# Optimization experiments

Measured on AMD Instinct MI355X. Metric: run time of the kernel, lower is better.

## Reference

```python
import jax, jax.numpy as jnp
import numpy as np
from jax import lax

B, N, D, E, P, K, H = 32, 512, 512, 8, 96, 25, 4
PAD = 12  # conv padding so length is preserved


def setup_inputs() -> dict:
    key = jax.random.key(0)
    ks = jax.random.split(key, 16)
    s = 0.05  # weight scale to keep softmax/cosine well-conditioned
    x = jax.random.normal(ks[0], (B, N, D), dtype=jnp.float32)
    router = jax.random.normal(ks[1], (1, E, D), dtype=jnp.float32)
    Wq = jax.random.normal(ks[2], (D, D), dtype=jnp.float32) * s
    bq = jax.random.normal(ks[3], (D,), dtype=jnp.float32) * s
    Wk = jax.random.normal(ks[4], (D, D), dtype=jnp.float32) * s
    bk = jax.random.normal(ks[5], (D,), dtype=jnp.float32) * s
    Wv = jax.random.normal(ks[6], (D, D), dtype=jnp.float32) * s
    bv = jax.random.normal(ks[7], (D,), dtype=jnp.float32) * s
    Wo = jax.random.normal(ks[8], (D, D), dtype=jnp.float32) * s
    bo = jax.random.normal(ks[9], (D,), dtype=jnp.float32) * s
    Wc = jax.random.normal(ks[10], (E, 2, K), dtype=jnp.float32) * s  # E experts' Conv1d(2,1,25) stacked as out-channels
    bc = jax.random.normal(ks[11], (E,), dtype=jnp.float32) * s
    Wp = jax.random.normal(ks[12], (E, D, P), dtype=jnp.float32) * s  # E experts' Linear(D,P), stored (in,out)
    bp = jax.random.normal(ks[13], (E, P), dtype=jnp.float32) * s
    return {"x": x, "router": router, "Wq": Wq, "bq": bq, "Wk": Wk, "bk": bk,
            "Wv": Wv, "bv": bv, "Wo": Wo, "bo": bo, "Wc": Wc, "bc": bc,
            "Wp": Wp, "bp": bp}


def _forward(x, router, Wq, bq, Wk, bk, Wv, bv, Wo, bo, Wc, bc, Wp, bp):
    b, n, d = x.shape
    e = router.shape[1]
    dk = d // H
    r = jnp.broadcast_to(router, (b, e, d))
    # multi-head attention: queries=router slots, keys/values=x (dropout = identity at eval)
    q = (r @ Wq + bq).reshape(b, e, H, dk)
    k = (x @ Wk + bk).reshape(b, n, H, dk)
    v = (x @ Wv + bv).reshape(b, n, H, dk)
    scale = 1.0 / jnp.sqrt(jnp.asarray(dk, x.dtype))
    scores = jnp.einsum('blhe,bshe->bhls', q, k)  # [b,H,e,n]
    A = jax.nn.softmax(scale * scores, axis=-1)
    att = jnp.einsum('bhls,bshd->blhd', A, v).reshape(b, e, d)
    att = att @ Wo + bo  # [b,e,d]
    # cosine-similarity routing score, mapped to (1+pi)/2
    dot = jnp.einsum('bed,bnd->ben', att, x)
    norm_a = jnp.linalg.norm(att, axis=2, keepdims=True)          # [b,e,1]
    norm_x = jnp.linalg.norm(x, axis=2)[:, None, :]                # [b,1,n]
    score = (1.0 + dot / (norm_a * norm_x)) / 2.0                  # [b,e,n]
    idx = jnp.argmax(score, axis=1)                                # [b,n] expert per token
    z = jnp.take_along_axis(att, idx[:, :, None], axis=1)          # [b,n,d]
    result = jnp.stack([x, z], axis=-2).reshape(b * n, 2, d)       # [bn,2,d]
    # run all E expert convs at once (experts stacked as output channels)
    conv_out = lax.conv_general_dilated(
        result, Wc, window_strides=(1,), padding=[(PAD, PAD)],
        dimension_numbers=('NCH', 'OIH', 'NCH')) + bc[None, :, None]  # [bn,E,d]
    lin = jnp.einsum('nel,elp->nep', conv_out, Wp) + bp[None]         # [bn,E,P]
    flat_idx = idx.reshape(-1)
    out = jnp.take_along_axis(lin, flat_idx[:, None, None], axis=1)[:, 0, :]
    return out.reshape(b, n, P)


def reference(x, router, Wq, bq, Wk, bk, Wv, bv, Wo, bo, Wc, bc, Wp, bp):
    return _forward(x, router, Wq, bq, Wk, bk, Wv, bv, Wo, bo, Wc, bc, Wp, bp)
```

## Files before the change

### kernel.cpp

```cpp
#include <hip/hip_runtime.h>
#include <hip/hip_bf16.h>

#define B_ 32
#define N_ 512
#define D_ 512
#define E_ 8
#define P_ 96
#define KC 25
#define H_ 4
#define DK 128
#define HE 32
#define BN 16384

typedef short short8 __attribute__((ext_vector_type(8)));
typedef float f32x4 __attribute__((ext_vector_type(4)));

#define OCNT  4096
#define OS2   4352
#define OM    5120
#define OC    21504
#define OA    21536
#define OATT  676896
#define OTOK  807968
#define OWEFF 939040
#define OZC   1332256
#define OUP   1356832
#define OA1   5551136

__device__ __forceinline__ float b2f(short s) {
  unsigned u = ((unsigned)(unsigned short)s) << 16;
  return __builtin_bit_cast(float, u);
}
__device__ __forceinline__ unsigned short f2b(float f) {
  return __builtin_bit_cast(unsigned short, __float2bfloat16(f));
}

__global__ __launch_bounds__(256) void k_head(const float* __restrict__ router,
        const float* __restrict__ Wq, const float* __restrict__ bq,
        const float* __restrict__ Wk, const float* __restrict__ bk,
        const float* __restrict__ Wp, const float* __restrict__ Wc,
        float* __restrict__ M, float* __restrict__ c,
        int* __restrict__ cnt, float* __restrict__ s2,
        __hip_bfloat16* __restrict__ weff) {
  __shared__ float sm[5824];
  int bid = blockIdx.x;
  int tid = threadIdx.x;
  if (bid < 64) {
    float* rs = sm;
    float* ps = sm + 512;
    float* qs = sm + 768;
    int he = bid >> 1, ch = bid & 1;
    int h = he >> 3, e = he & 7;
    for (int i = tid; i < 512; i += 256) rs[i] = router[e * D_ + i];
    __syncthreads();
    {
      int j = tid & 127, dh = tid >> 7;
      const float* wq = Wq + h * 128 + j;
      float acc = 0.f;
      for (int d = dh * 256; d < dh * 256 + 256; d += 4) {
        acc = fmaf(rs[d], wq[d * D_], acc);
        acc = fmaf(rs[d + 1], wq[(d + 1) * D_], acc);
        acc = fmaf(rs[d + 2], wq[(d + 2) * D_], acc);
        acc = fmaf(rs[d + 3], wq[(d + 3) * D_], acc);
      }
      ps[dh * 128 + j] = acc;
    }
    __syncthreads();
    if (tid < 128) qs[tid] = ps[tid] + ps[128 + tid] + bq[h * 128 + tid];
    __syncthreads();
    {
      int d0 = ch * 256 + tid;
      const float* wrow = Wk + d0 * D_ + h * 128;
      float acc = 0.f;
      for (int jj = 0; jj < 128; jj += 4) {
        float4 wv = *(const float4*)(wrow + jj);
        acc = fmaf(wv.x, qs[jj], acc);
        acc = fmaf(wv.y, qs[jj + 1], acc);
        acc = fmaf(wv.z, qs[jj + 2], acc);
        acc = fmaf(wv.w, qs[jj + 3], acc);
      }
      M[he * D_ + d0] = acc;
    }
    if (ch == 0 && tid < 64) {
      float s = qs[tid] * bk[h * 128 + tid] + qs[tid + 64] * bk[h * 128 + tid + 64];
#pragma unroll
      for (int off = 32; off; off >>= 1) s += __shfl_xor(s, off);
      if (tid == 0) c[he] = s;
    }
  } else if (bid < 192) {
    float* T = sm;
    float* wcs = sm + 5760;
    int eb = bid - 64;
    int e = eb >> 4, mc = eb & 15;
    int lo = mc * 32 - 12;
    for (int idx = tid; idx < 56 * 24; idx += 256) {
      int lp = idx / 24, p4 = (idx - lp * 24) * 4;
      int l = lo + lp;
      float4 v = {0.f, 0.f, 0.f, 0.f};
      if (l >= 0 && l < D_) v = *(const float4*)(Wp + (e * D_ + l) * P_ + p4);
      T[p4 * 60 + lp] = v.x; T[(p4 + 1) * 60 + lp] = v.y;
      T[(p4 + 2) * 60 + lp] = v.z; T[(p4 + 3) * 60 + lp] = v.w;
    }
    if (tid < 50) wcs[tid] = Wc[e * 2 * KC + tid];
    __syncthreads();
    int m = tid & 31, pg = tid >> 5;
#pragma unroll
    for (int j = 0; j < 2; ++j)
      for (int k2 = 0; k2 < 12; ++k2) {
        int p = pg * 12 + k2;
        float acc = 0.f;
#pragma unroll
        for (int k = 0; k < KC; ++k)
          acc = fmaf(wcs[j * 25 + k], T[p * 60 + m - k + 24], acc);
        weff[(((e * 2 + j) * P_ + p) << 9) + mc * 32 + m] = __float2bfloat16(acc);
      }
  } else {
    int e = bid - 192;
    if (bid == 192) cnt[tid] = 0;
    if (tid < 192) {
      int p = tid % 96, lg = tid / 96;
      float s = 0.f;
      const float* wp = Wp + e * D_ * P_ + p;
      for (int l = lg * 256; l < lg * 256 + 256; ++l) s += wp[l * P_];
      sm[lg * 96 + p] = s;
    }
    __syncthreads();
    if (tid < 96) s2[e * 96 + tid] = sm[tid] + sm[96 + tid];
  }
}

__global__ __launch_bounds__(128) void k_logits(const float* __restrict__ x,
        const float* __restrict__ M, float* __restrict__ A0,
        float* __restrict__ A1) {
  __shared__ float xs[64 * 132];
  __shared__ float Ms[32 * 132];
  int dh = blockIdx.x & 1;
  int nt8 = (blockIdx.x >> 1) & 7;
  int b = blockIdx.x >> 4;
  int tid = threadIdx.x;
  const float* xb = x + (b * N_ + nt8 * 64) * D_ + dh * 256;
  const float* Mb = M + dh * 256;
  float acc[4][4] = {{0.f}};
  for (int kc = 0; kc < 2; ++kc) {
    for (int idx = tid; idx < 2048; idx += 128) {
      int r = idx >> 5, c4 = (idx & 31) * 4;
      *(float4*)(xs + r * 132 + c4) = *(const float4*)(xb + r * D_ + kc * 128 + c4);
    }
    for (int idx = tid; idx < 1024; idx += 128) {
      int r = idx >> 5, c4 = (idx & 31) * 4;
      *(float4*)(Ms + r * 132 + c4) = *(const float4*)(Mb + r * D_ + kc * 128 + c4);
    }
    __syncthreads();
    int nt = tid & 15, ht = tid >> 4;
#pragma unroll 4
    for (int d4 = 0; d4 < 128; d4 += 4) {
      float4 xv[4], mv[4];
#pragma unroll
      for (int i = 0; i < 4; ++i)
        xv[i] = *(const float4*)(xs + (nt + 16 * i) * 132 + d4);
#pragma unroll
      for (int j = 0; j < 4; ++j)
        mv[j] = *(const float4*)(Ms + (ht + 8 * j) * 132 + d4);
#pragma unroll
      for (int i = 0; i < 4; ++i)
#pragma unroll
        for (int j = 0; j < 4; ++j) {
          float s = acc[i][j];
          s = fmaf(xv[i].x, mv[j].x, s);
          s = fmaf(xv[i].y, mv[j].y, s);
          s = fmaf(xv[i].z, mv[j].z, s);
          s = fmaf(xv[i].w, mv[j].w, s);
          acc[i][j] = s;
        }
    }
    __syncthreads();
  }
  int nt = tid & 15, ht = tid >> 4;
  float* Ad = dh ? A1 : A0;
#pragma unroll
  for (int j = 0; j < 4; ++j) {
    int he = ht + 8 * j;
#pragma unroll
    for (int i = 0; i < 4; ++i)
      Ad[(b * HE + he) * N_ + nt8 * 64 + nt + 16 * i] = acc[i][j];
  }
}

__global__ __launch_bounds__(512) void k_u3(const float* __restrict__ x,
        const float* __restrict__ A0, const float* __restrict__ A1,
        const float* __restrict__ c, float* __restrict__ up) {
  __shared__ float As[64 * 33];
  __shared__ float mS[32], sS[32];
  int nq = blockIdx.x, b = blockIdx.y;
  int tid = threadIdx.x;
  const float scale = 0.08838834764831845f;
  {
    int wv = tid >> 6, lane = tid & 63;
    int he = wv * 4 + (lane >> 4);
    int l16 = lane & 15;
    const float* r0 = A0 + (b * HE + he) * N_;
    const float* r1 = A1 + (b * HE + he) * N_;
    float cc = c[he];
    float v[32];
    float m = -1e30f;
#pragma unroll
    for (int k = 0; k < 32; ++k) {
      int n = l16 + k * 16;
      float vv = scale * (r0[n] + r1[n] + cc);
      v[k] = vv;
      m = fmaxf(m, vv);
    }
    m = fmaxf(m, __shfl_xor(m, 1)); m = fmaxf(m, __shfl_xor(m, 2));
    m = fmaxf(m, __shfl_xor(m, 4)); m = fmaxf(m, __shfl_xor(m, 8));
    float s = 0.f;
#pragma unroll
    for (int k = 0; k < 32; ++k) s += expf(v[k] - m);
    s += __shfl_xor(s, 1); s += __shfl_xor(s, 2);
    s += __shfl_xor(s, 4); s += __shfl_xor(s, 8);
    if (l16 == 0) { mS[he] = m; sS[he] = 1.0f / s; }
  }
  __syncthreads();
  for (int idx = tid; idx < 64 * 32; idx += 512) {
    int n = idx & 63, he = idx >> 6;
    int gn = nq * 64 + n;
    float vv = scale * (A0[(b * HE + he) * N_ + gn] + A1[(b * HE + he) * N_ + gn]
                        + c[he]);
    As[n * 33 + he] = expf(vv - mS[he]) * sS[he];
  }
  __syncthreads();
  int dq = tid & 127, hg = tid >> 7;
  const float* xb = x + (b * N_ + nq * 64) * D_ + dq * 4;
  float acc[8][4];
#pragma unroll
  for (int j = 0; j < 8; ++j)
#pragma unroll
    for (int k = 0; k < 4; ++k) acc[j][k] = 0.f;
  for (int n = 0; n < 64; ++n) {
    float4 xv = *(const float4*)(xb + n * D_);
    const float* ar = As + n * 33 + hg * 8;
#pragma unroll
    for (int j = 0; j < 8; ++j) {
      float a = ar[j];
      acc[j][0] = fmaf(a, xv.x, acc[j][0]);
      acc[j][1] = fmaf(a, xv.y, acc[j][1]);
      acc[j][2] = fmaf(a, xv.z, acc[j][2]);
      acc[j][3] = fmaf(a, xv.w, acc[j][3]);
    }
  }
  float* o = up + (((b * 8 + nq) * HE) + hg * 8) * D_ + dq * 4;
#pragma unroll
  for (int j = 0; j < 8; ++j) {
    float4 v; v.x = acc[j][0]; v.y = acc[j][1]; v.z = acc[j][2]; v.w = acc[j][3];
    *(float4*)(o + j * D_) = v;
  }
}

__global__ __launch_bounds__(512) void k_vo3(const float* __restrict__ up,
        const float* __restrict__ Wv, const float* __restrict__ bv,
        const float* __restrict__ Wo, const float* __restrict__ bo,
        float* __restrict__ att) {
  __shared__ float us[4 * 512];
  __shared__ float part[4 * 512];
  __shared__ float ap_s[512];
  int b = blockIdx.x >> 3, e = blockIdx.x & 7;
  int tid = threadIdx.x;
  for (int idx = tid; idx < 4 * 128; idx += 512) {
    int h = idx >> 7, d4 = (idx & 127) * 4;
    const float* base = up + ((b * 8) * HE + h * 8 + e) * D_ + d4;
    float4 s = {0.f, 0.f, 0.f, 0.f};
#pragma unroll
    for (int nq = 0; nq < 8; ++nq) {
      float4 v = *(const float4*)(base + nq * HE * D_);
      s.x += v.x; s.y += v.y; s.z += v.z; s.w += v.w;
    }
    *(float4*)(us + h * 512 + d4) = s;
  }
  __syncthreads();
  {
    int cch = tid >> 7, j = tid & 127;
    int i0 = j * 4;
    int h = j >> 5;
    const float* ur = us + h * 512;
    const float* wv = Wv + i0;
    float4 acc = {0.f, 0.f, 0.f, 0.f};
    int d0 = cch * 128;
#pragma unroll 4
    for (int d = d0; d < d0 + 128; ++d) {
      float4 wq = *(const float4*)(wv + d * D_);
      float a = ur[d];
      acc.x = fmaf(a, wq.x, acc.x);
      acc.y = fmaf(a, wq.y, acc.y);
      acc.z = fmaf(a, wq.z, acc.z);
      acc.w = fmaf(a, wq.w, acc.w);
    }
    *(float4*)(part + cch * 512 + i0) = acc;
  }
  __syncthreads();
  ap_s[tid] = part[tid] + part[512 + tid] + part[1024 + tid] + part[1536 + tid]
              + bv[tid];
  __syncthreads();
  {
    int cch = tid >> 7, j = tid & 127;
    int o0 = j * 4;
    const float* wo = Wo + o0;
    float4 acc = {0.f, 0.f, 0.f, 0.f};
    int i0 = cch * 128;
#pragma unroll 4
    for (int i = i0; i < i0 + 128; ++i) {
      float4 wq = *(const float4*)(wo + i * D_);
      float a = ap_s[i];
      acc.x = fmaf(a, wq.x, acc.x);
      acc.y = fmaf(a, wq.y, acc.y);
      acc.z = fmaf(a, wq.z, acc.z);
      acc.w = fmaf(a, wq.w, acc.w);
    }
    *(float4*)(part + cch * 512 + o0) = acc;
  }
  __syncthreads();
  att[(b * E_ + e) * D_ + tid] = part[tid] + part[512 + tid] + part[1024 + tid]
                                 + part[1536 + tid] + bo[tid];
}

__global__ __launch_bounds__(256) void k_route2(const float* __restrict__ x,
        const float* __restrict__ att, const __hip_bfloat16* __restrict__ weff,
        const float* __restrict__ s2, const float* __restrict__ bc,
        const float* __restrict__ bp, int* __restrict__ cnt,
        int* __restrict__ tok, float* __restrict__ zc) {
  __shared__ float att_s[8 * D_];
  __shared__ float rn[8];
  __shared__ float red[4][520];
  __shared__ int blist[8][32];
  __shared__ int bcnt[8];
  int b = blockIdx.x >> 4, tile = blockIdx.x & 15;
  for (int idx = threadIdx.x; idx < 1024; idx += 256)
    *(float4*)(att_s + idx * 4) = *(const float4*)(att + b * E_ * D_ + idx * 4);
  if (threadIdx.x < 8) bcnt[threadIdx.x] = 0;
  __syncthreads();
  {
    int e = threadIdx.x >> 5, l = threadIdx.x & 31;
    float s = 0.f;
    for (int d0 = l; d0 < D_; d0 += 32) {
      float v = att_s[e * D_ + d0];
      s = fmaf(v, v, s);
    }
#pragma unroll
    for (int off = 16; off; off >>= 1) s += __shfl_xor(s, off);
    if (l == 0) rn[e] = 1.0f / sqrtf(s);
  }
  __syncthreads();
  int w = threadIdx.x >> 6, lane = threadIdx.x & 63;
  int e2 = lane & 7, ch = lane >> 3;
  float* rw = red[w];
  for (int i = 0; i < 8; ++i) {
    int t = b * N_ + tile * 32 + w * 8 + i;
    const float* xp = x + t * D_ + lane * 8;
    float4 xa = *(const float4*)xp;
    float4 xb4 = *(const float4*)(xp + 4);
    float p[8];
#pragma unroll
    for (int e = 0; e < 8; ++e) {
      const float* apt = att_s + e * D_ + lane * 8;
      float4 a0 = *(const float4*)apt;
      float4 a1 = *(const float4*)(apt + 4);
      float s = a0.x * xa.x;
      s = fmaf(a0.y, xa.y, s); s = fmaf(a0.z, xa.z, s); s = fmaf(a0.w, xa.w, s);
      s = fmaf(a1.x, xb4.x, s); s = fmaf(a1.y, xb4.y, s);
      s = fmaf(a1.z, xb4.z, s); s = fmaf(a1.w, xb4.w, s);
      p[e] = s;
    }
#pragma unroll
    for (int e = 0; e < 8; ++e) rw[e * 65 + lane] = p[e];
    float s = 0.f;
#pragma unroll
    for (int k = 0; k < 8; ++k) s += rw[e2 * 65 + ch * 8 + k];
    s += __shfl_xor(s, 8); s += __shfl_xor(s, 16); s += __shfl_xor(s, 32);
    float sc = s * rn[e2];
    int be = e2;
#pragma unroll
    for (int off = 1; off < 8; off <<= 1) {
      float o = __shfl_xor(sc, off);
      int oe = __shfl_xor(be, off);
      if (o > sc || (o == sc && oe < be)) { sc = o; be = oe; }
    }
    if (lane == 0) {
      int slot = atomicAdd(&bcnt[be], 1);
      blist[be][slot] = t;
    }
  }
  __syncthreads();
  {
    int e = threadIdx.x >> 5, r = threadIdx.x & 31;
    int ce = bcnt[e];
    int gs = 0;
    if (r == 0 && ce > 0) gs = atomicAdd(&cnt[e * 32], ce);
    gs = __shfl(gs, (threadIdx.x & 63) & 32);
    for (int k2 = r; k2 < ce; k2 += 32) tok[e * BN + gs + k2] = blist[e][k2];
  }
  int grp = threadIdx.x >> 4, l16 = threadIdx.x & 15;
  for (int r = 0; r < 3; ++r) {
    int P = tile * 48 + r * 16 + grp;
    int ez = P / 96, p = P - ez * 96;
    const short* wrow = (const short*)weff + (((ez * 2 + 1) * P_ + p) << 9);
    const float* arow = att_s + ez * D_;
    float acc = 0.f;
#pragma unroll
    for (int seg = 0; seg < 4; ++seg) {
      int d = seg * 128 + l16 * 8;
      short8 w8 = *(const short8*)(wrow + d);
      const float* a8 = arow + d;
      acc = fmaf(a8[0], b2f(w8[0]), acc); acc = fmaf(a8[1], b2f(w8[1]), acc);
      acc = fmaf(a8[2], b2f(w8[2]), acc); acc = fmaf(a8[3], b2f(w8[3]), acc);
      acc = fmaf(a8[4], b2f(w8[4]), acc); acc = fmaf(a8[5], b2f(w8[5]), acc);
      acc = fmaf(a8[6], b2f(w8[6]), acc); acc = fmaf(a8[7], b2f(w8[7]), acc);
    }
    acc += __shfl_xor(acc, 1); acc += __shfl_xor(acc, 2);
    acc += __shfl_xor(acc, 4); acc += __shfl_xor(acc, 8);
    if (l16 == 0)
      zc[(b * E_ + ez) * P_ + p] = acc + bc[ez] * s2[ez * 96 + p] + bp[ez * 96 + p];
  }
}

__global__ __launch_bounds__(256) void k_final(const float* __restrict__ x,
        const __hip_bfloat16* __restrict__ weff, const float* __restrict__ zc,
        const int* __restrict__ cnt, const int* __restrict__ tok,
        float* __restrict__ out) {
  __shared__ __align__(16) unsigned short xsb[32 * 520];
  __shared__ int toks[32];
  int g = blockIdx.x;
  int cl_e[E_], bs[E_ + 1];
  bs[0] = 0;
#pragma unroll
  for (int e = 0; e < E_; ++e) {
    cl_e[e] = cnt[e * 32];
    bs[e + 1] = bs[e] + ((cl_e[e] + 31) >> 5);
  }
  if (g >= bs[E_]) return;
  int e = 0;
#pragma unroll
  for (int k = 1; k < E_; ++k) if (g >= bs[k]) e = k;
  int base = (g - bs[e]) * 32;
  int cnt_e = cl_e[e];
  int cl = cnt_e - base; if (cl > 32) cl = 32;
  int tid = threadIdx.x;
  if (tid < 32) toks[tid] = (tid < cl) ? tok[e * BN + base + tid] : tok[e * BN + base];
  __syncthreads();
  for (int idx = tid; idx < 32 * 128; idx += 256) {
    int r = idx >> 7, c4 = (idx & 127) * 4;
    float4 v = *(const float4*)(x + toks[r] * D_ + c4);
    ushort4 u4;
    u4.x = f2b(v.x); u4.y = f2b(v.y); u4.z = f2b(v.z); u4.w = f2b(v.w);
    *(ushort4*)(xsb + r * 520 + c4) = u4;
  }
  __syncthreads();
  int wave = tid >> 6, lane = tid & 63;
  int mw = wave & 1, nw = wave >> 1;
  int m16 = lane & 15, quad = lane >> 4;
  const short* w0 = (const short*)(weff + (e * 2 + 0) * P_ * D_);
  f32x4 acc[3];
#pragma unroll
  for (int nt = 0; nt < 3; ++nt) acc[nt] = (f32x4){0.f, 0.f, 0.f, 0.f};
  const short* arow = (const short*)xsb + (mw * 16 + m16) * 520 + quad * 8;
  const short* brow = w0 + (nw * 48 + m16) * D_ + quad * 8;
  for (int kt = 0; kt < 16; ++kt) {
    int koff = kt * 32;
    short8 a = *(const short8*)(arow + koff);
#pragma unroll
    for (int nt = 0; nt < 3; ++nt) {
      short8 bf = *(const short8*)(brow + nt * 16 * D_ + koff);
      acc[nt] = __builtin_amdgcn_mfma_f32_16x16x32_bf16(a, bf, acc[nt], 0, 0, 0);
    }
  }
#pragma unroll
  for (int nt = 0; nt < 3; ++nt)
#pragma unroll
    for (int rr = 0; rr < 4; ++rr) {
      int row = mw * 16 + quad * 4 + rr;
      if (row < cl) {
        int tg = toks[row];
        int bb = tg >> 9;
        int p = nw * 48 + nt * 16 + m16;
        out[tg * P_ + p] = acc[nt][rr] + zc[(bb * E_ + e) * P_ + p];
      }
    }
}

extern "C" void kernel_launch(void* const* d_in, const int* in_sizes, int n_in,
                              void* d_out, int out_size, void* d_ws, size_t ws_size,
                              hipStream_t stream) {
  const float* x      = (const float*)d_in[0];
  const float* router = (const float*)d_in[1];
  const float* Wq     = (const float*)d_in[2];
  const float* bq     = (const float*)d_in[3];
  const float* Wk     = (const float*)d_in[4];
  const float* bk     = (const float*)d_in[5];
  const float* Wv     = (const float*)d_in[6];
  const float* bv     = (const float*)d_in[7];
  const float* Wo     = (const float*)d_in[8];
  const float* bo     = (const float*)d_in[9];
  const float* Wc     = (const float*)d_in[10];
  const float* bc     = (const float*)d_in[11];
  const float* Wp     = (const float*)d_in[12];
  const float* bp     = (const float*)d_in[13];
  float* out = (float*)d_out;
  float* w = (float*)d_ws;

  int*   cnt  = (int*)(w + OCNT);
  float* s2   = w + OS2;
  float* M    = w + OM;
  float* c    = w + OC;
  float* A0   = w + OA;
  float* A1   = w + OA1;
  float* att  = w + OATT;
  int*   tok  = (int*)(w + OTOK);
  __hip_bfloat16* weff = (__hip_bfloat16*)(w + OWEFF);
  float* zc   = w + OZC;
  float* up   = w + OUP;

  k_head<<<200, 256, 0, stream>>>(router, Wq, bq, Wk, bk, Wp, Wc, M, c, cnt, s2, weff);
  k_logits<<<512, 128, 0, stream>>>(x, M, A0, A1);
  k_u3<<<dim3(8, 32), 512, 0, stream>>>(x, A0, A1, c, up);
  k_vo3<<<256, 512, 0, stream>>>(up, Wv, bv, Wo, bo, att);
  k_route2<<<512, 256, 0, stream>>>(x, att, weff, s2, bc, bp, cnt, tok, zc);
  k_final<<<520, 256, 0, stream>>>(x, weff, zc, cnt, tok, out);
}
```

Measured before the change: 223.2 us.

## Split V/O projection into two kernels that reuse weight loads across experts

The fused per-(batch,expert) V and O projection kernel is replaced by two kernels, each handling all 8 experts of a batch for one 128-column slice. Every Wv/Wo element loaded is now reused across 8 experts held in registers, so weight traffic drops roughly eightfold. The cost is an extra kernel launch and a round trip of the intermediate through global memory, which reuses the A0 workspace region. The grid also shrinks from 256 blocks to 128 blocks of 256 threads, which lowers occupancy.

```diff
diff --git a/kernel.cpp b/kernel.cpp
--- a/kernel.cpp
+++ b/kernel.cpp
@@ -255,70 +255,141 @@
   }
 }
 
-__global__ __launch_bounds__(512) void k_vo3(const float* __restrict__ up,
+__global__ __launch_bounds__(256) void k_voa(const float* __restrict__ up,
         const float* __restrict__ Wv, const float* __restrict__ bv,
-        const float* __restrict__ Wo, const float* __restrict__ bo,
-        float* __restrict__ att) {
-  __shared__ float us[4 * 512];
-  __shared__ float part[4 * 512];
-  __shared__ float ap_s[512];
-  int b = blockIdx.x >> 3, e = blockIdx.x & 7;
+        float* __restrict__ ap) {
+  __shared__ float us8[8][520];
+  __shared__ float pr[8192];
+  int b = blockIdx.x >> 2, h = blockIdx.x & 3;
   int tid = threadIdx.x;
-  for (int idx = tid; idx < 4 * 128; idx += 512) {
-    int h = idx >> 7, d4 = (idx & 127) * 4;
-    const float* base = up + ((b * 8) * HE + h * 8 + e) * D_ + d4;
+  for (int idx = tid; idx < 1024; idx += 256) {
+    int e = idx >> 7, d4 = (idx & 127) * 4;
+    const float* base = up + (((b * 8) * HE) + h * 8 + e) * D_ + d4;
     float4 s = {0.f, 0.f, 0.f, 0.f};
 #pragma unroll
     for (int nq = 0; nq < 8; ++nq) {
       float4 v = *(const float4*)(base + nq * HE * D_);
       s.x += v.x; s.y += v.y; s.z += v.z; s.w += v.w;
     }
-    *(float4*)(us + h * 512 + d4) = s;
+    *(float4*)(&us8[e][d4]) = s;
+  }
+  __syncthreads();
+  int cg = tid & 31, kk = tid >> 5;
+  int c0 = h * 128 + cg * 4;
+  float acc[8][4];
+#pragma unroll
+  for (int e = 0; e < 8; ++e)
+#pragma unroll
+    for (int j = 0; j < 4; ++j) acc[e][j] = 0.f;
+  for (int d = kk * 64; d < kk * 64 + 64; d += 4) {
+    float4 w0 = *(const float4*)(Wv + (d + 0) * D_ + c0);
+    float4 w1 = *(const float4*)(Wv + (d + 1) * D_ + c0);
+    float4 w2 = *(const float4*)(Wv + (d + 2) * D_ + c0);
+    float4 w3 = *(const float4*)(Wv + (d + 3) * D_ + c0);
+#pragma unroll
+    for (int e = 0; e < 8; ++e) {
+      float4 u = *(const float4*)(&us8[e][d]);
+      acc[e][0] = fmaf(u.x, w0.x, acc[e][0]);
+      acc[e][0] = fmaf(u.y, w1.x, acc[e][0]);
+      acc[e][0] = fmaf(u.z, w2.x, acc[e][0]);
+      acc[e][0] = fmaf(u.w, w3.x, acc[e][0]);
+      acc[e][1] = fmaf(u.x, w0.y, acc[e][1]);
+      acc[e][1] = fmaf(u.y, w1.y, acc[e][1]);
+      acc[e][1] = fmaf(u.z, w2.y, acc[e][1]);
+      acc[e][1] = fmaf(u.w, w3.y, acc[e][1]);
+      acc[e][2] = fmaf(u.x, w0.z, acc[e][2]);
+      acc[e][2] = fmaf(u.y, w1.z, acc[e][2]);
+      acc[e][2] = fmaf(u.z, w2.z, acc[e][2]);
+      acc[e][2] = fmaf(u.w, w3.z, acc[e][2]);
+      acc[e][3] = fmaf(u.x, w0.w, acc[e][3]);
+      acc[e][3] = fmaf(u.y, w1.w, acc[e][3]);
+      acc[e][3] = fmaf(u.z, w2.w, acc[e][3]);
+      acc[e][3] = fmaf(u.w, w3.w, acc[e][3]);
+    }
+  }
+#pragma unroll
+  for (int e = 0; e < 8; ++e) {
+    float4 v; v.x = acc[e][0]; v.y = acc[e][1]; v.z = acc[e][2]; v.w = acc[e][3];
+    *(float4*)(&pr[kk * 1024 + e * 128 + cg * 4]) = v;
   }
   __syncthreads();
   {
-    int cch = tid >> 7, j = tid & 127;
-    int i0 = j * 4;
-    int h = j >> 5;
-    const float* ur = us + h * 512;
-    const float* wv = Wv + i0;
-    float4 acc = {0.f, 0.f, 0.f, 0.f};
-    int d0 = cch * 128;
-#pragma unroll 4
-    for (int d = d0; d < d0 + 128; ++d) {
-      float4 wq = *(const float4*)(wv + d * D_);
-      float a = ur[d];
-      acc.x = fmaf(a, wq.x, acc.x);
-      acc.y = fmaf(a, wq.y, acc.y);
-      acc.z = fmaf(a, wq.z, acc.z);
-      acc.w = fmaf(a, wq.w, acc.w);
-    }
-    *(float4*)(part + cch * 512 + i0) = acc;
-  }
-  __syncthreads();
-  ap_s[tid] = part[tid] + part[512 + tid] + part[1024 + tid] + part[1536 + tid]
-              + bv[tid];
+    int e = tid >> 5, cc = (tid & 31) * 4;
+    float4 s = *(const float4*)(&pr[tid * 4]);
+#pragma unroll
+    for (int k = 1; k < 8; ++k) {
+      float4 p = *(const float4*)(&pr[k * 1024 + tid * 4]);
+      s.x += p.x; s.y += p.y; s.z += p.z; s.w += p.w;
+    }
+    float4 bb = *(const float4*)(bv + h * 128 + cc);
+    s.x += bb.x; s.y += bb.y; s.z += bb.z; s.w += bb.w;
+    *(float4*)(ap + (b * 8 + e) * D_ + h * 128 + cc) = s;
+  }
+}
+
+__global__ __launch_bounds__(256) void k_vob(const float* __restrict__ ap,
+        const float* __restrict__ Wo, const float* __restrict__ bo,
+        float* __restrict__ att) {
+  __shared__ float ap8[8][520];
+  __shared__ float pr[8192];
+  int b = blockIdx.x >> 2, cq = blockIdx.x & 3;
+  int tid = threadIdx.x;
+  for (int idx = tid; idx < 1024; idx += 256) {
+    int e = idx >> 7, i4 = (idx & 127) * 4;
+    *(float4*)(&ap8[e][i4]) = *(const float4*)(ap + (b * 8 + e) * D_ + i4);
+  }
+  __syncthreads();
+  int cg = tid & 31, kk = tid >> 5;
+  int c0 = cq * 128 + cg * 4;
+  float acc[8][4];
+#pragma unroll
+  for (int e = 0; e < 8; ++e)
+#pragma unroll
+    for (int j = 0; j < 4; ++j) acc[e][j] = 0.f;
+  for (int i = kk * 64; i < kk * 64 + 64; i += 4) {
+    float4 w0 = *(const float4*)(Wo + (i + 0) * D_ + c0);
+    float4 w1 = *(const float4*)(Wo + (i + 1) * D_ + c0);
+    float4 w2 = *(const float4*)(Wo + (i + 2) * D_ + c0);
+    float4 w3 = *(const float4*)(Wo + (i + 3) * D_ + c0);
+#pragma unroll
+    for (int e = 0; e < 8; ++e) {
+      float4 u = *(const float4*)(&ap8[e][i]);
+      acc[e][0] = fmaf(u.x, w0.x, acc[e][0]);
+      acc[e][0] = fmaf(u.y, w1.x, acc[e][0]);
+      acc[e][0] = fmaf(u.z, w2.x, acc[e][0]);
+      acc[e][0] = fmaf(u.w, w3.x, acc[e][0]);
+      acc[e][1] = fmaf(u.x, w0.y, acc[e][1]);
+      acc[e][1] = fmaf(u.y, w1.y, acc[e][1]);
+      acc[e][1] = fmaf(u.z, w2.y, acc[e][1]);
+      acc[e][1] = fmaf(u.w, w3.y, acc[e][1]);
+      acc[e][2] = fmaf(u.x, w0.z, acc[e][2]);
+      acc[e][2] = fmaf(u.y, w1.z, acc[e][2]);
+      acc[e][2] = fmaf(u.z, w2.z, acc[e][2]);
+      acc[e][2] = fmaf(u.w, w3.z, acc[e][2]);
+      acc[e][3] = fmaf(u.x, w0.w, acc[e][3]);
+      acc[e][3] = fmaf(u.y, w1.w, acc[e][3]);
+      acc[e][3] = fmaf(u.z, w2.w, acc[e][3]);
+      acc[e][3] = fmaf(u.w, w3.w, acc[e][3]);
+    }
+  }
+#pragma unroll
+  for (int e = 0; e < 8; ++e) {
+    float4 v; v.x = acc[e][0]; v.y = acc[e][1]; v.z = acc[e][2]; v.w = acc[e][3];
+    *(float4*)(&pr[kk * 1024 + e * 128 + cg * 4]) = v;
+  }
   __syncthreads();
   {
-    int cch = tid >> 7, j = tid & 127;
-    int o0 = j * 4;
-    const float* wo = Wo + o0;
-    float4 acc = {0.f, 0.f, 0.f, 0.f};
-    int i0 = cch * 128;
-#pragma unroll 4
-    for (int i = i0; i < i0 + 128; ++i) {
-      float4 wq = *(const float4*)(wo + i * D_);
-      float a = ap_s[i];
-      acc.x = fmaf(a, wq.x, acc.x);
-      acc.y = fmaf(a, wq.y, acc.y);
-      acc.z = fmaf(a, wq.z, acc.z);
-      acc.w = fmaf(a, wq.w, acc.w);
-    }
-    *(float4*)(part + cch * 512 + o0) = acc;
-  }
-  __syncthreads();
-  att[(b * E_ + e) * D_ + tid] = part[tid] + part[512 + tid] + part[1024 + tid]
-                                 + part[1536 + tid] + bo[tid];
+    int e = tid >> 5, cc = (tid & 31) * 4;
+    float4 s = *(const float4*)(&pr[tid * 4]);
+#pragma unroll
+    for (int k = 1; k < 8; ++k) {
+      float4 p = *(const float4*)(&pr[k * 1024 + tid * 4]);
+      s.x += p.x; s.y += p.y; s.z += p.z; s.w += p.w;
+    }
+    float4 bb = *(const float4*)(bo + cq * 128 + cc);
+    s.x += bb.x; s.y += bb.y; s.z += bb.z; s.w += bb.w;
+    *(float4*)(att + (b * E_ + e) * D_ + cq * 128 + cc) = s;
+  }
 }
 
 __global__ __launch_bounds__(256) void k_route2(const float* __restrict__ x,
@@ -515,11 +586,13 @@
   __hip_bfloat16* weff = (__hip_bfloat16*)(w + OWEFF);
   float* zc   = w + OZC;
   float* up   = w + OUP;
+  float* ap   = w + OA;
 
   k_head<<<200, 256, 0, stream>>>(router, Wq, bq, Wk, bk, Wp, Wc, M, c, cnt, s2, weff);
   k_logits<<<512, 128, 0, stream>>>(x, M, A0, A1);
   k_u3<<<dim3(8, 32), 512, 0, stream>>>(x, A0, A1, c, up);
-  k_vo3<<<256, 512, 0, stream>>>(up, Wv, bv, Wo, bo, att);
+  k_voa<<<128, 256, 0, stream>>>(up, Wv, bv, ap);
+  k_vob<<<128, 256, 0, stream>>>(ap, Wo, bo, att);
   k_route2<<<512, 256, 0, stream>>>(x, att, weff, s2, bc, bp, cnt, tok, zc);
   k_final<<<520, 256, 0, stream>>>(x, weff, zc, cnt, tok, out);
 }
```

After: 224.7 us. No clear change (+0.7%).

## Fuse last four kernels into one cooperative kernel with grid syncs

Applied to the files above, without the earlier changes.

Merges the softmax-weighted sum, value/output projection, routing and expert-GEMM kernels into a single cooperative launch of 256 blocks of 512 threads. Phases are separated by grid-wide syncs and share one reused shared-memory buffer. The routing phase now handles 64 tokens per block instead of 32, and the final expert GEMM loops over groups with only four of eight waves doing MFMA. This removes three launch gaps in exchange for grid-sync cost, lower parallelism in some phases, and half-idle waves in the last phase.

```diff
diff --git a/kernel.cpp b/kernel.cpp
--- a/kernel.cpp
+++ b/kernel.cpp
@@ -1,5 +1,8 @@
 #include <hip/hip_runtime.h>
 #include <hip/hip_bf16.h>
+#include <hip/hip_cooperative_groups.h>
+
+namespace cg = cooperative_groups;
 
 #define B_ 32
 #define N_ 512
@@ -186,302 +189,311 @@
   }
 }
 
-__global__ __launch_bounds__(512) void k_u3(const float* __restrict__ x,
-        const float* __restrict__ A0, const float* __restrict__ A1,
-        const float* __restrict__ c, float* __restrict__ up) {
-  __shared__ float As[64 * 33];
-  __shared__ float mS[32], sS[32];
-  int nq = blockIdx.x, b = blockIdx.y;
-  int tid = threadIdx.x;
-  const float scale = 0.08838834764831845f;
-  {
-    int wv = tid >> 6, lane = tid & 63;
-    int he = wv * 4 + (lane >> 4);
-    int l16 = lane & 15;
-    const float* r0 = A0 + (b * HE + he) * N_;
-    const float* r1 = A1 + (b * HE + he) * N_;
-    float cc = c[he];
-    float v[32];
-    float m = -1e30f;
-#pragma unroll
-    for (int k = 0; k < 32; ++k) {
-      int n = l16 + k * 16;
-      float vv = scale * (r0[n] + r1[n] + cc);
-      v[k] = vv;
-      m = fmaxf(m, vv);
-    }
-    m = fmaxf(m, __shfl_xor(m, 1)); m = fmaxf(m, __shfl_xor(m, 2));
-    m = fmaxf(m, __shfl_xor(m, 4)); m = fmaxf(m, __shfl_xor(m, 8));
-    float s = 0.f;
-#pragma unroll
-    for (int k = 0; k < 32; ++k) s += expf(v[k] - m);
-    s += __shfl_xor(s, 1); s += __shfl_xor(s, 2);
-    s += __shfl_xor(s, 4); s += __shfl_xor(s, 8);
-    if (l16 == 0) { mS[he] = m; sS[he] = 1.0f / s; }
-  }
-  __syncthreads();
-  for (int idx = tid; idx < 64 * 32; idx += 512) {
-    int n = idx & 63, he = idx >> 6;
-    int gn = nq * 64 + n;
-    float vv = scale * (A0[(b * HE + he) * N_ + gn] + A1[(b * HE + he) * N_ + gn]
-                        + c[he]);
-    As[n * 33 + he] = expf(vv - mS[he]) * sS[he];
-  }
-  __syncthreads();
-  int dq = tid & 127, hg = tid >> 7;
-  const float* xb = x + (b * N_ + nq * 64) * D_ + dq * 4;
-  float acc[8][4];
-#pragma unroll
-  for (int j = 0; j < 8; ++j)
-#pragma unroll
-    for (int k = 0; k < 4; ++k) acc[j][k] = 0.f;
-  for (int n = 0; n < 64; ++n) {
-    float4 xv = *(const float4*)(xb + n * D_);
-    const float* ar = As + n * 33 + hg * 8;
-#pragma unroll
-    for (int j = 0; j < 8; ++j) {
-      float a = ar[j];
-      acc[j][0] = fmaf(a, xv.x, acc[j][0]);
-      acc[j][1] = fmaf(a, xv.y, acc[j][1]);
-      acc[j][2] = fmaf(a, xv.z, acc[j][2]);
-      acc[j][3] = fmaf(a, xv.w, acc[j][3]);
-    }
-  }
-  float* o = up + (((b * 8 + nq) * HE) + hg * 8) * D_ + dq * 4;
-#pragma unroll
-  for (int j = 0; j < 8; ++j) {
-    float4 v; v.x = acc[j][0]; v.y = acc[j][1]; v.z = acc[j][2]; v.w = acc[j][3];
-    *(float4*)(o + j * D_) = v;
-  }
-}
-
-__global__ __launch_bounds__(512) void k_vo3(const float* __restrict__ up,
+__global__ __launch_bounds__(512, 2) void k_mega(
+        const float* __restrict__ x, const float* __restrict__ A0,
+        const float* __restrict__ A1, const float* __restrict__ c,
+        float* __restrict__ up,
         const float* __restrict__ Wv, const float* __restrict__ bv,
         const float* __restrict__ Wo, const float* __restrict__ bo,
-        float* __restrict__ att) {
-  __shared__ float us[4 * 512];
-  __shared__ float part[4 * 512];
-  __shared__ float ap_s[512];
-  int b = blockIdx.x >> 3, e = blockIdx.x & 7;
+        float* __restrict__ att,
+        const __hip_bfloat16* __restrict__ weff, const float* __restrict__ s2,
+        const float* __restrict__ bc, const float* __restrict__ bp,
+        int* __restrict__ cnt, int* __restrict__ tok, float* __restrict__ zc,
+        float* __restrict__ out) {
+  __shared__ __align__(16) char smem[35200];
+  cg::grid_group grid = cg::this_grid();
   int tid = threadIdx.x;
-  for (int idx = tid; idx < 4 * 128; idx += 512) {
-    int h = idx >> 7, d4 = (idx & 127) * 4;
-    const float* base = up + ((b * 8) * HE + h * 8 + e) * D_ + d4;
-    float4 s = {0.f, 0.f, 0.f, 0.f};
-#pragma unroll
-    for (int nq = 0; nq < 8; ++nq) {
-      float4 v = *(const float4*)(base + nq * HE * D_);
-      s.x += v.x; s.y += v.y; s.z += v.z; s.w += v.w;
-    }
-    *(float4*)(us + h * 512 + d4) = s;
-  }
-  __syncthreads();
+
   {
-    int cch = tid >> 7, j = tid & 127;
-    int i0 = j * 4;
-    int h = j >> 5;
-    const float* ur = us + h * 512;
-    const float* wv = Wv + i0;
-    float4 acc = {0.f, 0.f, 0.f, 0.f};
-    int d0 = cch * 128;
+    float* As = (float*)smem;
+    float* mS = (float*)(smem + 8448);
+    float* sS = (float*)(smem + 8576);
+    int nq = blockIdx.x & 7, b = blockIdx.x >> 3;
+    const float scale = 0.08838834764831845f;
+    {
+      int wv = tid >> 6, lane = tid & 63;
+      int he = wv * 4 + (lane >> 4);
+      int l16 = lane & 15;
+      const float* r0 = A0 + (b * HE + he) * N_;
+      const float* r1 = A1 + (b * HE + he) * N_;
+      float cc = c[he];
+      float v[32];
+      float m = -1e30f;
+#pragma unroll
+      for (int k = 0; k < 32; ++k) {
+        int n = l16 + k * 16;
+        float vv = scale * (r0[n] + r1[n] + cc);
+        v[k] = vv;
+        m = fmaxf(m, vv);
+      }
+      m = fmaxf(m, __shfl_xor(m, 1)); m = fmaxf(m, __shfl_xor(m, 2));
+      m = fmaxf(m, __shfl_xor(m, 4)); m = fmaxf(m, __shfl_xor(m, 8));
+      float s = 0.f;
+#pragma unroll
+      for (int k = 0; k < 32; ++k) s += expf(v[k] - m);
+      s += __shfl_xor(s, 1); s += __shfl_xor(s, 2);
+      s += __shfl_xor(s, 4); s += __shfl_xor(s, 8);
+      if (l16 == 0) { mS[he] = m; sS[he] = 1.0f / s; }
+    }
+    __syncthreads();
+    for (int idx = tid; idx < 64 * 32; idx += 512) {
+      int n = idx & 63, he = idx >> 6;
+      int gn = nq * 64 + n;
+      float vv = scale * (A0[(b * HE + he) * N_ + gn] + A1[(b * HE + he) * N_ + gn]
+                          + c[he]);
+      As[n * 33 + he] = expf(vv - mS[he]) * sS[he];
+    }
+    __syncthreads();
+    int dq = tid & 127, hg = tid >> 7;
+    const float* xb = x + (b * N_ + nq * 64) * D_ + dq * 4;
+    float acc[8][4];
+#pragma unroll
+    for (int j = 0; j < 8; ++j)
+#pragma unroll
+      for (int k = 0; k < 4; ++k) acc[j][k] = 0.f;
+    for (int n = 0; n < 64; ++n) {
+      float4 xv = *(const float4*)(xb + n * D_);
+      const float* ar = As + n * 33 + hg * 8;
+#pragma unroll
+      for (int j = 0; j < 8; ++j) {
+        float a = ar[j];
+        acc[j][0] = fmaf(a, xv.x, acc[j][0]);
+        acc[j][1] = fmaf(a, xv.y, acc[j][1]);
+        acc[j][2] = fmaf(a, xv.z, acc[j][2]);
+        acc[j][3] = fmaf(a, xv.w, acc[j][3]);
+      }
+    }
+    float* o = up + (((b * 8 + nq) * HE) + hg * 8) * D_ + dq * 4;
+#pragma unroll
+    for (int j = 0; j < 8; ++j) {
+      float4 v; v.x = acc[j][0]; v.y = acc[j][1]; v.z = acc[j][2]; v.w = acc[j][3];
+      *(float4*)(o + j * D_) = v;
+    }
+  }
+  grid.sync();
+
+  {
+    float* us   = (float*)smem;
+    float* part = (float*)(smem + 8192);
+    float* ap_s = (float*)(smem + 16384);
+    int b = blockIdx.x >> 3, e = blockIdx.x & 7;
+    for (int idx = tid; idx < 4 * 128; idx += 512) {
+      int h = idx >> 7, d4 = (idx & 127) * 4;
+      const float* base = up + ((b * 8) * HE + h * 8 + e) * D_ + d4;
+      float4 s = {0.f, 0.f, 0.f, 0.f};
+#pragma unroll
+      for (int nq = 0; nq < 8; ++nq) {
+        float4 v = *(const float4*)(base + nq * HE * D_);
+        s.x += v.x; s.y += v.y; s.z += v.z; s.w += v.w;
+      }
+      *(float4*)(us + h * 512 + d4) = s;
+    }
+    __syncthreads();
+    {
+      int cch = tid >> 7, j = tid & 127;
+      int i0 = j * 4;
+      int h = j >> 5;
+      const float* ur = us + h * 512;
+      const float* wv = Wv + i0;
+      float4 acc = {0.f, 0.f, 0.f, 0.f};
+      int d0 = cch * 128;
 #pragma unroll 4
-    for (int d = d0; d < d0 + 128; ++d) {
-      float4 wq = *(const float4*)(wv + d * D_);
-      float a = ur[d];
-      acc.x = fmaf(a, wq.x, acc.x);
-      acc.y = fmaf(a, wq.y, acc.y);
-      acc.z = fmaf(a, wq.z, acc.z);
-      acc.w = fmaf(a, wq.w, acc.w);
-    }
-    *(float4*)(part + cch * 512 + i0) = acc;
-  }
-  __syncthreads();
-  ap_s[tid] = part[tid] + part[512 + tid] + part[1024 + tid] + part[1536 + tid]
-              + bv[tid];
-  __syncthreads();
+      for (int d = d0; d < d0 + 128; ++d) {
+        float4 wq = *(const float4*)(wv + d * D_);
+        float a = ur[d];
+        acc.x = fmaf(a, wq.x, acc.x);
+        acc.y = fmaf(a, wq.y, acc.y);
+        acc.z = fmaf(a, wq.z, acc.z);
+        acc.w = fmaf(a, wq.w, acc.w);
+      }
+      *(float4*)(part + cch * 512 + i0) = acc;
+    }
+    __syncthreads();
+    ap_s[tid] = part[tid] + part[512 + tid] + part[1024 + tid] + part[1536 + tid]
+                + bv[tid];
+    __syncthreads();
+    {
+      int cch = tid >> 7, j = tid & 127;
+      int o0 = j * 4;
+      const float* wo = Wo + o0;
+      float4 acc = {0.f, 0.f, 0.f, 0.f};
+      int i0 = cch * 128;
+#pragma unroll 4
+      for (int i = i0; i < i0 + 128; ++i) {
+        float4 wq = *(const float4*)(wo + i * D_);
+        float a = ap_s[i];
+        acc.x = fmaf(a, wq.x, acc.x);
+        acc.y = fmaf(a, wq.y, acc.y);
+        acc.z = fmaf(a, wq.z, acc.z);
+        acc.w = fmaf(a, wq.w, acc.w);
+      }
+      *(float4*)(part + cch * 512 + o0) = acc;
+    }
+    __syncthreads();
+    att[(b * E_ + e) * D_ + tid] = part[tid] + part[512 + tid] + part[1024 + tid]
+                                   + part[1536 + tid] + bo[tid];
+  }
+  grid.sync();
+
   {
-    int cch = tid >> 7, j = tid & 127;
-    int o0 = j * 4;
-    const float* wo = Wo + o0;
-    float4 acc = {0.f, 0.f, 0.f, 0.f};
-    int i0 = cch * 128;
-#pragma unroll 4
-    for (int i = i0; i < i0 + 128; ++i) {
-      float4 wq = *(const float4*)(wo + i * D_);
-      float a = ap_s[i];
-      acc.x = fmaf(a, wq.x, acc.x);
-      acc.y = fmaf(a, wq.y, acc.y);
-      acc.z = fmaf(a, wq.z, acc.z);
-      acc.w = fmaf(a, wq.w, acc.w);
-    }
-    *(float4*)(part + cch * 512 + o0) = acc;
-  }
-  __syncthreads();
-  att[(b * E_ + e) * D_ + tid] = part[tid] + part[512 + tid] + part[1024 + tid]
-                                 + part[1536 + tid] + bo[tid];
-}
-
-__global__ __launch_bounds__(256) void k_route2(const float* __restrict__ x,
-        const float* __restrict__ att, const __hip_bfloat16* __restrict__ weff,
-        const float* __restrict__ s2, const float* __restrict__ bc,
-        const float* __restrict__ bp, int* __restrict__ cnt,
-        int* __restrict__ tok, float* __restrict__ zc) {
-  __shared__ float att_s[8 * D_];
-  __shared__ float rn[8];
-  __shared__ float red[4][520];
-  __shared__ int blist[8][32];
-  __shared__ int bcnt[8];
-  int b = blockIdx.x >> 4, tile = blockIdx.x & 15;
-  for (int idx = threadIdx.x; idx < 1024; idx += 256)
-    *(float4*)(att_s + idx * 4) = *(const float4*)(att + b * E_ * D_ + idx * 4);
-  if (threadIdx.x < 8) bcnt[threadIdx.x] = 0;
-  __syncthreads();
+    float* att_s = (float*)smem;
+    float* rn    = (float*)(smem + 16384);
+    float* red   = (float*)(smem + 16416);
+    int*   blist = (int*)(smem + 33056);
+    int*   bcnt  = (int*)(smem + 35104);
+    int b = blockIdx.x >> 3, tile = blockIdx.x & 7;
+    for (int idx = tid; idx < 1024; idx += 512)
+      *(float4*)(att_s + idx * 4) = *(const float4*)(att + b * E_ * D_ + idx * 4);
+    if (tid < 8) bcnt[tid] = 0;
+    __syncthreads();
+    if (tid < 256) {
+      int e = tid >> 5, l = tid & 31;
+      float s = 0.f;
+      for (int d0 = l; d0 < D_; d0 += 32) {
+        float v = att_s[e * D_ + d0];
+        s = fmaf(v, v, s);
+      }
+#pragma unroll
+      for (int off = 16; off; off >>= 1) s += __shfl_xor(s, off);
+      if (l == 0) rn[e] = 1.0f / sqrtf(s);
+    }
+    __syncthreads();
+    int w = tid >> 6, lane = tid & 63;
+    int e2 = lane & 7, ch = lane >> 3;
+    float* rw = red + w * 520;
+    for (int i = 0; i < 8; ++i) {
+      int t = b * N_ + tile * 64 + w * 8 + i;
+      const float* xp = x + t * D_ + lane * 8;
+      float4 xa = *(const float4*)xp;
+      float4 xb4 = *(const float4*)(xp + 4);
+      float p[8];
+#pragma unroll
+      for (int e = 0; e < 8; ++e) {
+        const float* apt = att_s + e * D_ + lane * 8;
+        float4 a0 = *(const float4*)apt;
+        float4 a1 = *(const float4*)(apt + 4);
+        float s = a0.x * xa.x;
+        s = fmaf(a0.y, xa.y, s); s = fmaf(a0.z, xa.z, s); s = fmaf(a0.w, xa.w, s);
+        s = fmaf(a1.x, xb4.x, s); s = fmaf(a1.y, xb4.y, s);
+        s = fmaf(a1.z, xb4.z, s); s = fmaf(a1.w, xb4.w, s);
+        p[e] = s;
+      }
+#pragma unroll
+      for (int e = 0; e < 8; ++e) rw[e * 65 + lane] = p[e];
+      float s = 0.f;
+#pragma unroll
+      for (int k = 0; k < 8; ++k) s += rw[e2 * 65 + ch * 8 + k];
+      s += __shfl_xor(s, 8); s += __shfl_xor(s, 16); s += __shfl_xor(s, 32);
+      float sc = s * rn[e2];
+      int be = e2;
+#pragma unroll
+      for (int off = 1; off < 8; off <<= 1) {
+        float o = __shfl_xor(sc, off);
+        int oe = __shfl_xor(be, off);
+        if (o > sc || (o == sc && oe < be)) { sc = o; be = oe; }
+      }
+      if (lane == 0) {
+        int slot = atomicAdd(&bcnt[be], 1);
+        blist[be * 64 + slot] = t;
+      }
+    }
+    __syncthreads();
+    if (tid < 256) {
+      int e = tid >> 5, r = tid & 31;
+      int ce = bcnt[e];
+      int gs = 0;
+      if (r == 0 && ce > 0) gs = atomicAdd(&cnt[e * 32], ce);
+      gs = __shfl(gs, (tid & 63) & 32);
+      for (int k2 = r; k2 < ce; k2 += 32) tok[e * BN + gs + k2] = blist[e * 64 + k2];
+    }
+    int grp = tid >> 4, l16 = tid & 15;
+    int ez = tile;
+    const float* arow = att_s + ez * D_;
+    for (int r = 0; r < 3; ++r) {
+      int p = r * 32 + grp;
+      const short* wrow = (const short*)weff + (((ez * 2 + 1) * P_ + p) << 9);
+      float acc = 0.f;
+#pragma unroll
+      for (int seg = 0; seg < 4; ++seg) {
+        int d = seg * 128 + l16 * 8;
+        short8 w8 = *(const short8*)(wrow + d);
+        const float* a8 = arow + d;
+        acc = fmaf(a8[0], b2f(w8[0]), acc); acc = fmaf(a8[1], b2f(w8[1]), acc);
+        acc = fmaf(a8[2], b2f(w8[2]), acc); acc = fmaf(a8[3], b2f(w8[3]), acc);
+        acc = fmaf(a8[4], b2f(w8[4]), acc); acc = fmaf(a8[5], b2f(w8[5]), acc);
+        acc = fmaf(a8[6], b2f(w8[6]), acc); acc = fmaf(a8[7], b2f(w8[7]), acc);
+      }
+      acc += __shfl_xor(acc, 1); acc += __shfl_xor(acc, 2);
+      acc += __shfl_xor(acc, 4); acc += __shfl_xor(acc, 8);
+      if (l16 == 0)
+        zc[(b * E_ + ez) * P_ + p] = acc + bc[ez] * s2[ez * 96 + p] + bp[ez * 96 + p];
+    }
+  }
+  grid.sync();
+
   {
-    int e = threadIdx.x >> 5, l = threadIdx.x & 31;
-    float s = 0.f;
-    for (int d0 = l; d0 < D_; d0 += 32) {
-      float v = att_s[e * D_ + d0];
-      s = fmaf(v, v, s);
-    }
-#pragma unroll
-    for (int off = 16; off; off >>= 1) s += __shfl_xor(s, off);
-    if (l == 0) rn[e] = 1.0f / sqrtf(s);
-  }
-  __syncthreads();
-  int w = threadIdx.x >> 6, lane = threadIdx.x & 63;
-  int e2 = lane & 7, ch = lane >> 3;
-  float* rw = red[w];
-  for (int i = 0; i < 8; ++i) {
-    int t = b * N_ + tile * 32 + w * 8 + i;
-    const float* xp = x + t * D_ + lane * 8;
-    float4 xa = *(const float4*)xp;
-    float4 xb4 = *(const float4*)(xp + 4);
-    float p[8];
-#pragma unroll
-    for (int e = 0; e < 8; ++e) {
-      const float* apt = att_s + e * D_ + lane * 8;
-      float4 a0 = *(const float4*)apt;
-      float4 a1 = *(const float4*)(apt + 4);
-      float s = a0.x * xa.x;
-      s = fmaf(a0.y, xa.y, s); s = fmaf(a0.z, xa.z, s); s = fmaf(a0.w, xa.w, s);
-      s = fmaf(a1.x, xb4.x, s); s = fmaf(a1.y, xb4.y, s);
-      s = fmaf(a1.z, xb4.z, s); s = fmaf(a1.w, xb4.w, s);
-      p[e] = s;
-    }
-#pragma unroll
-    for (int e = 0; e < 8; ++e) rw[e * 65 + lane] = p[e];
-    float s = 0.f;
-#pragma unroll
-    for (int k = 0; k < 8; ++k) s += rw[e2 * 65 + ch * 8 + k];
-    s += __shfl_xor(s, 8); s += __shfl_xor(s, 16); s += __shfl_xor(s, 32);
-    float sc = s * rn[e2];
-    int be = e2;
-#pragma unroll
-    for (int off = 1; off < 8; off <<= 1) {
-      float o = __shfl_xor(sc, off);
-      int oe = __shfl_xor(be, off);
-      if (o > sc || (o == sc && oe < be)) { sc = o; be = oe; }
-    }
-    if (lane == 0) {
-      int slot = atomicAdd(&bcnt[be], 1);
-      blist[be][slot] = t;
-    }
-  }
-  __syncthreads();
-  {
-    int e = threadIdx.x >> 5, r = threadIdx.x & 31;
-    int ce = bcnt[e];
-    int gs = 0;
-    if (r == 0 && ce > 0) gs = atomicAdd(&cnt[e * 32], ce);
-    gs = __shfl(gs, (threadIdx.x & 63) & 32);
-    for (int k2 = r; k2 < ce; k2 += 32) tok[e * BN + gs + k2] = blist[e][k2];
-  }
-  int grp = threadIdx.x >> 4, l16 = threadIdx.x & 15;
-  for (int r = 0; r < 3; ++r) {
-    int P = tile * 48 + r * 16 + grp;
-    int ez = P / 96, p = P - ez * 96;
-    const short* wrow = (const short*)weff + (((ez * 2 + 1) * P_ + p) << 9);
-    const float* arow = att_s + ez * D_;
-    float acc = 0.f;
-#pragma unroll
-    for (int seg = 0; seg < 4; ++seg) {
-      int d = seg * 128 + l16 * 8;
-      short8 w8 = *(const short8*)(wrow + d);
-      const float* a8 = arow + d;
-      acc = fmaf(a8[0], b2f(w8[0]), acc); acc = fmaf(a8[1], b2f(w8[1]), acc);
-      acc = fmaf(a8[2], b2f(w8[2]), acc); acc = fmaf(a8[3], b2f(w8[3]), acc);
-      acc = fmaf(a8[4], b2f(w8[4]), acc); acc = fmaf(a8[5], b2f(w8[5]), acc);
-      acc = fmaf(a8[6], b2f(w8[6]), acc); acc = fmaf(a8[7], b2f(w8[7]), acc);
-    }
-    acc += __shfl_xor(acc, 1); acc += __shfl_xor(acc, 2);
-    acc += __shfl_xor(acc, 4); acc += __shfl_xor(acc, 8);
-    if (l16 == 0)
-      zc[(b * E_ + ez) * P_ + p] = acc + bc[ez] * s2[ez * 96 + p] + bp[ez * 96 + p];
-  }
-}
-
-__global__ __launch_bounds__(256) void k_final(const float* __restrict__ x,
-        const __hip_bfloat16* __restrict__ weff, const float* __restrict__ zc,
-        const int* __restrict__ cnt, const int* __restrict__ tok,
-        float* __restrict__ out) {
-  __shared__ __align__(16) unsigned short xsb[32 * 520];
-  __shared__ int toks[32];
-  int g = blockIdx.x;
-  int cl_e[E_], bs[E_ + 1];
-  bs[0] = 0;
-#pragma unroll
-  for (int e = 0; e < E_; ++e) {
-    cl_e[e] = cnt[e * 32];
-    bs[e + 1] = bs[e] + ((cl_e[e] + 31) >> 5);
-  }
-  if (g >= bs[E_]) return;
-  int e = 0;
-#pragma unroll
-  for (int k = 1; k < E_; ++k) if (g >= bs[k]) e = k;
-  int base = (g - bs[e]) * 32;
-  int cnt_e = cl_e[e];
-  int cl = cnt_e - base; if (cl > 32) cl = 32;
-  int tid = threadIdx.x;
-  if (tid < 32) toks[tid] = (tid < cl) ? tok[e * BN + base + tid] : tok[e * BN + base];
-  __syncthreads();
-  for (int idx = tid; idx < 32 * 128; idx += 256) {
-    int r = idx >> 7, c4 = (idx & 127) * 4;
-    float4 v = *(const float4*)(x + toks[r] * D_ + c4);
-    ushort4 u4;
-    u4.x = f2b(v.x); u4.y = f2b(v.y); u4.z = f2b(v.z); u4.w = f2b(v.w);
-    *(ushort4*)(xsb + r * 520 + c4) = u4;
-  }
-  __syncthreads();
-  int wave = tid >> 6, lane = tid & 63;
-  int mw = wave & 1, nw = wave >> 1;
-  int m16 = lane & 15, quad = lane >> 4;
-  const short* w0 = (const short*)(weff + (e * 2 + 0) * P_ * D_);
-  f32x4 acc[3];
-#pragma unroll
-  for (int nt = 0; nt < 3; ++nt) acc[nt] = (f32x4){0.f, 0.f, 0.f, 0.f};
-  const short* arow = (const short*)xsb + (mw * 16 + m16) * 520 + quad * 8;
-  const short* brow = w0 + (nw * 48 + m16) * D_ + quad * 8;
-  for (int kt = 0; kt < 16; ++kt) {
-    int koff = kt * 32;
-    short8 a = *(const short8*)(arow + koff);
-#pragma unroll
-    for (int nt = 0; nt < 3; ++nt) {
-      short8 bf = *(const short8*)(brow + nt * 16 * D_ + koff);
-      acc[nt] = __builtin_amdgcn_mfma_f32_16x16x32_bf16(a, bf, acc[nt], 0, 0, 0);
-    }
-  }
-#pragma unroll
-  for (int nt = 0; nt < 3; ++nt)
-#pragma unroll
-    for (int rr = 0; rr < 4; ++rr) {
-      int row = mw * 16 + quad * 4 + rr;
-      if (row < cl) {
-        int tg = toks[row];
-        int bb = tg >> 9;
-        int p = nw * 48 + nt * 16 + m16;
-        out[tg * P_ + p] = acc[nt][rr] + zc[(bb * E_ + e) * P_ + p];
-      }
-    }
+    unsigned short* xsb = (unsigned short*)smem;
+    int* toks = (int*)(smem + 33280);
+    int cl_e[E_], bs[E_ + 1];
+    bs[0] = 0;
+#pragma unroll
+    for (int e = 0; e < E_; ++e) {
+      cl_e[e] = cnt[e * 32];
+      bs[e + 1] = bs[e] + ((cl_e[e] + 31) >> 5);
+    }
+    int nb = bs[E_];
+    for (int g = blockIdx.x; g < nb; g += 256) {
+      int e = 0;
+#pragma unroll
+      for (int k = 1; k < E_; ++k) if (g >= bs[k]) e = k;
+      int base = (g - bs[e]) * 32;
+      int cnt_e = cl_e[e];
+      int cl = cnt_e - base; if (cl > 32) cl = 32;
+      if (tid < 32) toks[tid] = (tid < cl) ? tok[e * BN + base + tid] : tok[e * BN + base];
+      __syncthreads();
+      for (int idx = tid; idx < 32 * 128; idx += 512) {
+        int r = idx >> 7, c4 = (idx & 127) * 4;
+        float4 v = *(const float4*)(x + toks[r] * D_ + c4);
+        ushort4 u4;
+        u4.x = f2b(v.x); u4.y = f2b(v.y); u4.z = f2b(v.z); u4.w = f2b(v.w);
+        *(ushort4*)(xsb + r * 520 + c4) = u4;
+      }
+      __syncthreads();
+      int wave = tid >> 6, lane = tid & 63;
+      if (wave < 4) {
+        int mw = wave & 1, nw = wave >> 1;
+        int m16 = lane & 15, quad = lane >> 4;
+        const short* w0 = (const short*)(weff + (e * 2 + 0) * P_ * D_);
+        f32x4 acc[3];
+#pragma unroll
+        for (int nt = 0; nt < 3; ++nt) acc[nt] = (f32x4){0.f, 0.f, 0.f, 0.f};
+        const short* arow = (const short*)xsb + (mw * 16 + m16) * 520 + quad * 8;
+        const short* brow = w0 + (nw * 48 + m16) * D_ + quad * 8;
+        for (int kt = 0; kt < 16; ++kt) {
+          int koff = kt * 32;
+          short8 a = *(const short8*)(arow + koff);
+#pragma unroll
+          for (int nt = 0; nt < 3; ++nt) {
+            short8 bf = *(const short8*)(brow + nt * 16 * D_ + koff);
+            acc[nt] = __builtin_amdgcn_mfma_f32_16x16x32_bf16(a, bf, acc[nt], 0, 0, 0);
+          }
+        }
+#pragma unroll
+        for (int nt = 0; nt < 3; ++nt)
+#pragma unroll
+          for (int rr = 0; rr < 4; ++rr) {
+            int row = mw * 16 + quad * 4 + rr;
+            if (row < cl) {
+              int tg = toks[row];
+              int bb = tg >> 9;
+              int p = nw * 48 + nt * 16 + m16;
+              out[tg * P_ + p] = acc[nt][rr] + zc[(bb * E_ + e) * P_ + p];
+            }
+          }
+      }
+      __syncthreads();
+    }
+  }
 }
 
 extern "C" void kernel_launch(void* const* d_in, const int* in_sizes, int n_in,
@@ -518,8 +530,21 @@
 
   k_head<<<200, 256, 0, stream>>>(router, Wq, bq, Wk, bk, Wp, Wc, M, c, cnt, s2, weff);
   k_logits<<<512, 128, 0, stream>>>(x, M, A0, A1);
-  k_u3<<<dim3(8, 32), 512, 0, stream>>>(x, A0, A1, c, up);
-  k_vo3<<<256, 512, 0, stream>>>(up, Wv, bv, Wo, bo, att);
-  k_route2<<<512, 256, 0, stream>>>(x, att, weff, s2, bc, bp, cnt, tok, zc);
-  k_final<<<520, 256, 0, stream>>>(x, weff, zc, cnt, tok, out);
+
+  {
+    const float* xa = x;
+    const float* A0a = A0; const float* A1a = A1; const float* ca = c;
+    float* upa = up;
+    const float* Wva = Wv; const float* bva = bv;
+    const float* Woa = Wo; const float* boa = bo;
+    float* atta = att;
+    const __hip_bfloat16* weffa = weff; const float* s2a = s2;
+    const float* bca = bc; const float* bpa = bp;
+    int* cnta = cnt; int* toka = tok; float* zca = zc;
+    float* outa = out;
+    void* args[] = {&xa, &A0a, &A1a, &ca, &upa, &Wva, &bva, &Woa, &boa, &atta,
+                    &weffa, &s2a, &bca, &bpa, &cnta, &toka, &zca, &outa};
+    hipLaunchCooperativeKernel(reinterpret_cast<void*>(k_mega), dim3(256),
+                               dim3(512), args, 0, stream);
+  }
 }
```

New measurement: 343.6 us. 1.54x slower.
